# Kernel optimization log

Measured on AMD Instinct MI355X. Metric: run time of the kernel, lower is better.

## Reference

```python
import jax, jax.numpy as jnp
import numpy as np

B, N, K, D = 256, 100, 16, 128


def setup_inputs() -> dict:
    key = jax.random.key(0)
    k1, k2, k3, k4, k5, k6, k7 = jax.random.split(key, 7)
    return {
        "self_vectors": jax.random.normal(k1, (B, N, D), jnp.float32),
        "neighbor_vector": jax.random.normal(k2, (B, N, K, D), jnp.float32),
        "neighbor_weight": jax.random.uniform(k3, (B, N, K), jnp.float32),
        "extra_vector": jax.random.normal(k4, (B, N, D), jnp.float32),
        "w_1": jax.random.normal(k5, (D + 1, D), jnp.float32) / np.sqrt(D + 1),
        "w_2": jax.random.normal(k6, (D, 1), jnp.float32) / np.sqrt(D),
        "w_3": jax.random.normal(k7, (2 * D, D), jnp.float32) / np.sqrt(2 * D),
        "batch_size": B,
    }


def reference(self_vectors, neighbor_vector, neighbor_weight, extra_vector, w_1, w_2, w_3, batch_size):
    # attention branch (extra_vector is not None)
    feat = extra_vector[:, :, None, :] * neighbor_vector           # [B,N,K,D]
    feat = jnp.concatenate([feat, neighbor_weight[..., None]], -1)  # [B,N,K,D+1]
    alpha = jnp.einsum('bnkf,fd->bnkd', feat, w_1)                  # [B,N,K,D]
    alpha = jax.nn.leaky_relu(alpha, negative_slope=0.2)
    alpha = jnp.einsum('bnkd,do->bnk', alpha, w_2)                  # [B,N,K]
    alpha = jax.nn.softmax(alpha, axis=-1)[..., None]               # [B,N,K,1]
    agg = jnp.sum(alpha * neighbor_vector, axis=-2)                 # [B,N,D]
    # combine (dropout is identity in eval mode / p=0)
    out = jnp.concatenate([self_vectors, agg], axis=-1) @ w_3       # [B,N,D]
    out = out.reshape(batch_size, -1, w_3.shape[1])
    return jax.nn.relu(out)
```

## Files before the change

### kernel.cpp

```cpp
#include <hip/hip_runtime.h>
#include <stdint.h>

#define BN_TOTAL 25600
#define DDIM 128
#define KN 16

typedef __bf16 bf16x8 __attribute__((ext_vector_type(8)));
typedef __bf16 bf16x4 __attribute__((ext_vector_type(4)));
typedef float f32x4 __attribute__((ext_vector_type(4)));
typedef float f32x16 __attribute__((ext_vector_type(16)));

__device__ __forceinline__ void gload_lds16(const void* g, void* l) {
    __builtin_amdgcn_global_load_lds(
        (const __attribute__((address_space(1))) void*)g,
        (__attribute__((address_space(3))) void*)l, 16, 0, 0);
}

template<int CTRL>
__device__ __forceinline__ float rotadd(float v) {
    const int r = __builtin_amdgcn_mov_dpp(__builtin_bit_cast(int, v), CTRL, 0xF, 0xF, false);
    return v + __builtin_bit_cast(float, r);
}
__device__ __forceinline__ float allreduce16(float v) {
    v = rotadd<0x121>(v);
    v = rotadd<0x122>(v);
    v = rotadd<0x124>(v);
    v = rotadd<0x128>(v);
    return v;
}

__global__ __launch_bounds__(256) void k0_build_frags(
    const float* __restrict__ w1,
    const float* __restrict__ w3,
    bf16x8* __restrict__ fw1,
    bf16x8* __restrict__ fw3)
{
    const int slot = blockIdx.x * 256 + threadIdx.x;
    if (slot < 2048) {
        const int idx  = slot >> 6;
        const int lane = slot & 63;
        const int t = idx >> 2, s = idx & 3;
        const int grp = lane >> 4, lr = lane & 15;
        const int fbase = grp * 8 + 32 * s;
        const int d = t * 16 + lr;
        bf16x8 tmp;
        #pragma unroll
        for (int j = 0; j < 8; ++j)
            tmp[j] = (__bf16)w1[(fbase + j) * DDIM + d];
        fw1[slot] = tmp;
    } else {
        const int q = slot - 2048;
        const int idx  = q >> 6;
        const int lane = q & 63;
        const int t = idx >> 3, s = idx & 7;
        const int grp = lane >> 4, lr = lane & 15;
        const int fbase = grp * 8 + 32 * s;
        const int d = t * 16 + lr;
        bf16x8 tmp;
        #pragma unroll
        for (int j = 0; j < 8; ++j)
            tmp[j] = (__bf16)w3[(fbase + j) * DDIM + d];
        fw3[q] = tmp;
    }
}

__global__ __launch_bounds__(512, 6) void k1_attn_agg(
    const float* __restrict__ nbr,
    const float* __restrict__ wgt,
    const float* __restrict__ extra,
    const float* __restrict__ w1,
    const float* __restrict__ w2,
    const bf16x8* __restrict__ fw1,
    unsigned short* __restrict__ aggb)
{
    __shared__ bf16x8 b1frag[32][64];
    __shared__ float2 wlw2[DDIM];
    __shared__ __align__(16) unsigned short alds[8][16];

    const int tid  = threadIdx.x;
    const int lane = tid & 63;
    const int wave = tid >> 6;
    const int grp  = lane >> 4;
    const int lr   = lane & 15;
    const int half = lane >> 5;
    const int col  = lane & 31;

    #pragma unroll
    for (int c = 0; c < 4; ++c)
        gload_lds16(fw1 + (wave * 4 + c) * 64 + lane, &b1frag[wave * 4 + c][0]);
    if (tid < DDIM)
        wlw2[tid] = make_float2(w1[DDIM * DDIM + tid], w2[tid]);
    __syncthreads();

    const int bn = blockIdx.x * 8 + wave;
    const float* nb = nbr   + (size_t)bn * (KN * DDIM);
    const float* ex = extra + (size_t)bn * DDIM;

    const float4 wv = *(const float4*)(wgt + (size_t)bn * KN + grp * 4);
    float w2v[8];
    f32x4 acc[8];
    #pragma unroll
    for (int t = 0; t < 8; ++t) {
        const float2 ww = wlw2[t * 16 + lr];
        w2v[t] = ww.y;
        acc[t][0] = wv.x * ww.x;
        acc[t][1] = wv.y * ww.x;
        acc[t][2] = wv.z * ww.x;
        acc[t][3] = wv.w * ww.x;
    }

    #pragma unroll
    for (int s = 0; s < 4; ++s) {
        const int f0 = grp * 8 + 32 * s;
        const float4 n0 = *(const float4*)(nb + lr * DDIM + f0);
        const float4 n1 = *(const float4*)(nb + lr * DDIM + f0 + 4);
        const float4 e0 = *(const float4*)(ex + f0);
        const float4 e1 = *(const float4*)(ex + f0 + 4);
        bf16x8 af;
        af[0] = (__bf16)(n0.x * e0.x); af[1] = (__bf16)(n0.y * e0.y);
        af[2] = (__bf16)(n0.z * e0.z); af[3] = (__bf16)(n0.w * e0.w);
        af[4] = (__bf16)(n1.x * e1.x); af[5] = (__bf16)(n1.y * e1.y);
        af[6] = (__bf16)(n1.z * e1.z); af[7] = (__bf16)(n1.w * e1.w);
        #pragma unroll
        for (int t = 0; t < 8; ++t)
            acc[t] = __builtin_amdgcn_mfma_f32_16x16x32_bf16(
                         af, b1frag[t * 4 + s][lane], acc[t], 0, 0, 0);
    }

    bf16x8 b2f[4];
    #pragma unroll
    for (int t = 0; t < 4; ++t)
        #pragma unroll
        for (int j = 0; j < 8; ++j)
            b2f[t][j] = (__bf16)nb[(half * 8 + j) * DDIM + t * 32 + col];

    float sum0 = 0.f, sum1 = 0.f, sum2 = 0.f, sum3 = 0.f;
    #pragma unroll
    for (int t = 0; t < 8; ++t) {
        float h;
        h = acc[t][0]; h = fmaxf(h, 0.2f * h); sum0 = fmaf(h, w2v[t], sum0);
        h = acc[t][1]; h = fmaxf(h, 0.2f * h); sum1 = fmaf(h, w2v[t], sum1);
        h = acc[t][2]; h = fmaxf(h, 0.2f * h); sum2 = fmaf(h, w2v[t], sum2);
        h = acc[t][3]; h = fmaxf(h, 0.2f * h); sum3 = fmaf(h, w2v[t], sum3);
    }
    sum0 = allreduce16(sum0);
    sum1 = allreduce16(sum1);
    sum2 = allreduce16(sum2);
    sum3 = allreduce16(sum3);

    float mx = fmaxf(fmaxf(sum0, sum1), fmaxf(sum2, sum3));
    mx = fmaxf(mx, __shfl_xor(mx, 16, 64));
    mx = fmaxf(mx, __shfl_xor(mx, 32, 64));
    const float ev0 = __expf(sum0 - mx);
    const float ev1 = __expf(sum1 - mx);
    const float ev2 = __expf(sum2 - mx);
    const float ev3 = __expf(sum3 - mx);
    float es = ev0 + ev1 + ev2 + ev3;
    es += __shfl_xor(es, 16, 64);
    es += __shfl_xor(es, 32, 64);
    const float inv = 1.0f / es;

    if (lr == 0) {
        bf16x4 av;
        av[0] = (__bf16)(ev0 * inv);
        av[1] = (__bf16)(ev1 * inv);
        av[2] = (__bf16)(ev2 * inv);
        av[3] = (__bf16)(ev3 * inv);
        *(bf16x4*)&alds[wave][grp * 4] = av;
    }
    const bf16x8 a2 = *(const bf16x8*)&alds[wave][half * 8];

    f32x16 z;
    #pragma unroll
    for (int i = 0; i < 16; ++i) z[i] = 0.f;

    unsigned short* ao = aggb + (size_t)bn * DDIM;
    #pragma unroll
    for (int t = 0; t < 4; ++t) {
        const f32x16 r = __builtin_amdgcn_mfma_f32_32x32x16_bf16(a2, b2f[t], z, 0, 0, 0);
        if ((t >> 1) == half) {
            const __bf16 rb = (__bf16)r[0];
            ao[t * 32 + col] = __builtin_bit_cast(unsigned short, rb);
        }
    }
}

__global__ __launch_bounds__(512, 4) void k2_out_gemm(
    const float* __restrict__ selfv,
    const unsigned short* __restrict__ aggb,
    const bf16x8* __restrict__ fw3,
    float* __restrict__ out)
{
    __shared__ bf16x8 w3frag[64][64];

    const int tid  = threadIdx.x;
    const int lane = tid & 63;
    const int wave = tid >> 6;
    const int grp  = lane >> 4;
    const int lr   = lane & 15;

    #pragma unroll
    for (int c = 0; c < 8; ++c)
        gload_lds16(fw3 + (wave * 8 + c) * 64 + lane, &w3frag[wave * 8 + c][0]);
    __syncthreads();

    const int rowbase = blockIdx.x * 128 + wave * 16;
    const int row = rowbase + lr;

    f32x4 acc[8];
    #pragma unroll
    for (int t = 0; t < 8; ++t) {
        acc[t][0] = 0.f; acc[t][1] = 0.f; acc[t][2] = 0.f; acc[t][3] = 0.f;
    }

    #pragma unroll
    for (int s = 0; s < 8; ++s) {
        bf16x8 af;
        if (s < 4) {
            const int f0 = grp * 8 + 32 * s;
            const float4 x0 = *(const float4*)(selfv + (size_t)row * DDIM + f0);
            const float4 x1 = *(const float4*)(selfv + (size_t)row * DDIM + f0 + 4);
            af[0] = (__bf16)x0.x; af[1] = (__bf16)x0.y;
            af[2] = (__bf16)x0.z; af[3] = (__bf16)x0.w;
            af[4] = (__bf16)x1.x; af[5] = (__bf16)x1.y;
            af[6] = (__bf16)x1.z; af[7] = (__bf16)x1.w;
        } else {
            const int f0 = grp * 8 + 32 * (s - 4);
            af = *(const bf16x8*)(aggb + (size_t)row * DDIM + f0);
        }
        #pragma unroll
        for (int t = 0; t < 8; ++t)
            acc[t] = __builtin_amdgcn_mfma_f32_16x16x32_bf16(
                         af, w3frag[t * 8 + s][lane], acc[t], 0, 0, 0);
    }

    #pragma unroll
    for (int t = 0; t < 8; ++t) {
        #pragma unroll
        for (int j = 0; j < 4; ++j) {
            const int r = rowbase + grp * 4 + j;
            out[(size_t)r * DDIM + t * 16 + lr] = fmaxf(acc[t][j], 0.0f);
        }
    }
}

extern "C" void kernel_launch(void* const* d_in, const int* in_sizes, int n_in,
                              void* d_out, int out_size, void* d_ws, size_t ws_size,
                              hipStream_t stream)
{
    const float* selfv = (const float*)d_in[0];
    const float* nbr   = (const float*)d_in[1];
    const float* wgt   = (const float*)d_in[2];
    const float* extra = (const float*)d_in[3];
    const float* w1    = (const float*)d_in[4];
    const float* w2    = (const float*)d_in[5];
    const float* w3    = (const float*)d_in[6];
    float* out = (float*)d_out;

    unsigned short* aggb = (unsigned short*)d_ws;
    bf16x8* fw1 = (bf16x8*)((char*)d_ws + (8u << 20));
    bf16x8* fw3 = (bf16x8*)((char*)d_ws + (8u << 20) + (128u << 10));

    hipLaunchKernelGGL(k0_build_frags, dim3(24), dim3(256), 0, stream, w1, w3, fw1, fw3);
    hipLaunchKernelGGL(k1_attn_agg, dim3(3200), dim3(512), 0, stream,
                       nbr, wgt, extra, w1, w2, fw1, aggb);
    hipLaunchKernelGGL(k2_out_gemm, dim3(200), dim3(512), 0, stream,
                       selfv, aggb, fw3, out);
}
```

Before: 72.85 us.

## Fuse output GEMM into attention-aggregation kernel via LDS staging

Merges the attention/aggregation kernel and the output GEMM into one kernel. Each block now keeps its 8 aggregated rows in LDS and runs the concat-GEMM with w3 directly, so the bf16 agg round trip through global memory and one launch go away. In exchange, each wave loads w3 fragments from global into registers, and the 16x16 MFMA handles only 8 valid rows, so half of its output is wasted. Launch bounds drop from 6 to 4 waves-per-EU occupancy, which may reduce latency hiding for the memory-bound neighbor loads.

```diff
diff --git a/kernel.cpp b/kernel.cpp
--- a/kernel.cpp
+++ b/kernel.cpp
@@ -4,6 +4,7 @@
 #define BN_TOTAL 25600
 #define DDIM 128
 #define KN 16
+#define AGP 136
 
 typedef __bf16 bf16x8 __attribute__((ext_vector_type(8)));
 typedef __bf16 bf16x4 __attribute__((ext_vector_type(4)));
@@ -64,18 +65,21 @@
     }
 }
 
-__global__ __launch_bounds__(512, 6) void k1_attn_agg(
+__global__ __launch_bounds__(512, 4) void k_fused(
     const float* __restrict__ nbr,
     const float* __restrict__ wgt,
     const float* __restrict__ extra,
     const float* __restrict__ w1,
     const float* __restrict__ w2,
+    const float* __restrict__ selfv,
     const bf16x8* __restrict__ fw1,
-    unsigned short* __restrict__ aggb)
+    const bf16x8* __restrict__ fw3,
+    float* __restrict__ out)
 {
     __shared__ bf16x8 b1frag[32][64];
     __shared__ float2 wlw2[DDIM];
     __shared__ __align__(16) unsigned short alds[8][16];
+    __shared__ __align__(16) unsigned short agg_lds[8][AGP];
 
     const int tid  = threadIdx.x;
     const int lane = tid & 63;
@@ -92,7 +96,8 @@
         wlw2[tid] = make_float2(w1[DDIM * DDIM + tid], w2[tid]);
     __syncthreads();
 
-    const int bn = blockIdx.x * 8 + wave;
+    const int bn8 = blockIdx.x * 8;
+    const int bn  = bn8 + wave;
     const float* nb = nbr   + (size_t)bn * (KN * DDIM);
     const float* ex = extra + (size_t)bn * DDIM;
 
@@ -174,72 +179,57 @@
     #pragma unroll
     for (int i = 0; i < 16; ++i) z[i] = 0.f;
 
-    unsigned short* ao = aggb + (size_t)bn * DDIM;
     #pragma unroll
     for (int t = 0; t < 4; ++t) {
         const f32x16 r = __builtin_amdgcn_mfma_f32_32x32x16_bf16(a2, b2f[t], z, 0, 0, 0);
         if ((t >> 1) == half) {
             const __bf16 rb = (__bf16)r[0];
-            ao[t * 32 + col] = __builtin_bit_cast(unsigned short, rb);
+            agg_lds[wave][t * 32 + col] = __builtin_bit_cast(unsigned short, rb);
         }
     }
-}
-
-__global__ __launch_bounds__(512, 4) void k2_out_gemm(
-    const float* __restrict__ selfv,
-    const unsigned short* __restrict__ aggb,
-    const bf16x8* __restrict__ fw3,
-    float* __restrict__ out)
-{
-    __shared__ bf16x8 w3frag[64][64];
-
-    const int tid  = threadIdx.x;
-    const int lane = tid & 63;
-    const int wave = tid >> 6;
-    const int grp  = lane >> 4;
-    const int lr   = lane & 15;
-
-    #pragma unroll
-    for (int c = 0; c < 8; ++c)
-        gload_lds16(fw3 + (wave * 8 + c) * 64 + lane, &w3frag[wave * 8 + c][0]);
+
+    const int arow = lane & 7;
+    const int kofs = grp * 8;
+    float4 sx[4][2];
+    #pragma unroll
+    for (int s = 0; s < 4; ++s) {
+        const float* sp = selfv + (size_t)(bn8 + arow) * DDIM + kofs + 32 * s;
+        sx[s][0] = *(const float4*)sp;
+        sx[s][1] = *(const float4*)(sp + 4);
+    }
+    bf16x8 wf[8];
+    {
+        const bf16x8* fp = fw3 + (size_t)(wave * 8) * 64 + lane;
+        #pragma unroll
+        for (int s = 0; s < 8; ++s)
+            wf[s] = fp[s * 64];
+    }
+
     __syncthreads();
 
-    const int rowbase = blockIdx.x * 128 + wave * 16;
-    const int row = rowbase + lr;
-
-    f32x4 acc[8];
-    #pragma unroll
-    for (int t = 0; t < 8; ++t) {
-        acc[t][0] = 0.f; acc[t][1] = 0.f; acc[t][2] = 0.f; acc[t][3] = 0.f;
-    }
-
-    #pragma unroll
-    for (int s = 0; s < 8; ++s) {
+    f32x4 acc2;
+    acc2[0] = 0.f; acc2[1] = 0.f; acc2[2] = 0.f; acc2[3] = 0.f;
+
+    #pragma unroll
+    for (int s = 0; s < 4; ++s) {
         bf16x8 af;
-        if (s < 4) {
-            const int f0 = grp * 8 + 32 * s;
-            const float4 x0 = *(const float4*)(selfv + (size_t)row * DDIM + f0);
-            const float4 x1 = *(const float4*)(selfv + (size_t)row * DDIM + f0 + 4);
-            af[0] = (__bf16)x0.x; af[1] = (__bf16)x0.y;
-            af[2] = (__bf16)x0.z; af[3] = (__bf16)x0.w;
-            af[4] = (__bf16)x1.x; af[5] = (__bf16)x1.y;
-            af[6] = (__bf16)x1.z; af[7] = (__bf16)x1.w;
-        } else {
-            const int f0 = grp * 8 + 32 * (s - 4);
-            af = *(const bf16x8*)(aggb + (size_t)row * DDIM + f0);
-        }
-        #pragma unroll
-        for (int t = 0; t < 8; ++t)
-            acc[t] = __builtin_amdgcn_mfma_f32_16x16x32_bf16(
-                         af, w3frag[t * 8 + s][lane], acc[t], 0, 0, 0);
-    }
-
-    #pragma unroll
-    for (int t = 0; t < 8; ++t) {
+        af[0] = (__bf16)sx[s][0].x; af[1] = (__bf16)sx[s][0].y;
+        af[2] = (__bf16)sx[s][0].z; af[3] = (__bf16)sx[s][0].w;
+        af[4] = (__bf16)sx[s][1].x; af[5] = (__bf16)sx[s][1].y;
+        af[6] = (__bf16)sx[s][1].z; af[7] = (__bf16)sx[s][1].w;
+        acc2 = __builtin_amdgcn_mfma_f32_16x16x32_bf16(af, wf[s], acc2, 0, 0, 0);
+    }
+    #pragma unroll
+    for (int s = 0; s < 4; ++s) {
+        const bf16x8 af = *(const bf16x8*)&agg_lds[arow][kofs + 32 * s];
+        acc2 = __builtin_amdgcn_mfma_f32_16x16x32_bf16(af, wf[4 + s], acc2, 0, 0, 0);
+    }
+
+    if (grp < 2) {
         #pragma unroll
         for (int j = 0; j < 4; ++j) {
-            const int r = rowbase + grp * 4 + j;
-            out[(size_t)r * DDIM + t * 16 + lr] = fmaxf(acc[t][j], 0.0f);
+            const int r = bn8 + grp * 4 + j;
+            out[(size_t)r * DDIM + wave * 16 + lr] = fmaxf(acc2[j], 0.0f);
         }
     }
 }
@@ -257,13 +247,10 @@
     const float* w3    = (const float*)d_in[6];
     float* out = (float*)d_out;
 
-    unsigned short* aggb = (unsigned short*)d_ws;
     bf16x8* fw1 = (bf16x8*)((char*)d_ws + (8u << 20));
     bf16x8* fw3 = (bf16x8*)((char*)d_ws + (8u << 20) + (128u << 10));
 
     hipLaunchKernelGGL(k0_build_frags, dim3(24), dim3(256), 0, stream, w1, w3, fw1, fw3);
-    hipLaunchKernelGGL(k1_attn_agg, dim3(3200), dim3(512), 0, stream,
-                       nbr, wgt, extra, w1, w2, fw1, aggb);
-    hipLaunchKernelGGL(k2_out_gemm, dim3(200), dim3(512), 0, stream,
-                       selfv, aggb, fw3, out);
-}
+    hipLaunchKernelGGL(k_fused, dim3(3200), dim3(512), 0, stream,
+                       nbr, wgt, extra, w1, w2, selfv, fw1, fw3, out);
+}
```

Measured after the change: 83.73 us. 1.15x slower.

## Pipeline neighbor tiles through double-buffered LDS with async global-to-LDS loads

Applied to the files above, without the earlier changes.

The attention kernel becomes persistent-style: each 2-wave block handles 10 (b,n) rows per wave and prefetches the next rows' neighbor, extra and weight data into a double-buffered, XOR-swizzled LDS buffer using async global_load_lds, gated by explicit vmcnt waits. The goal is to overlap the dominant HBM streaming of neighbor vectors with the MFMA and softmax work, where the old version issued dependent global loads per row. W1 fragments are now read straight from global memory (cache) rather than staged in LDS. The risks are fewer waves for latency hiding, correctness of the hand-written vmcnt counts, and the repeated global reads of fw1 fragments.

```diff
diff --git a/kernel.cpp b/kernel.cpp
--- a/kernel.cpp
+++ b/kernel.cpp
@@ -4,6 +4,7 @@
 #define BN_TOTAL 25600
 #define DDIM 128
 #define KN 16
+#define K1_ITERS 10
 
 typedef __bf16 bf16x8 __attribute__((ext_vector_type(8)));
 typedef __bf16 bf16x4 __attribute__((ext_vector_type(4)));
@@ -64,7 +65,7 @@
     }
 }
 
-__global__ __launch_bounds__(512, 6) void k1_attn_agg(
+__global__ __launch_bounds__(128) void k1_pipe(
     const float* __restrict__ nbr,
     const float* __restrict__ wgt,
     const float* __restrict__ extra,
@@ -73,9 +74,9 @@
     const bf16x8* __restrict__ fw1,
     unsigned short* __restrict__ aggb)
 {
-    __shared__ bf16x8 b1frag[32][64];
+    __shared__ float buf[2][2][2304];
     __shared__ float2 wlw2[DDIM];
-    __shared__ __align__(16) unsigned short alds[8][16];
+    __shared__ __align__(16) unsigned short alds[2][16];
 
     const int tid  = threadIdx.x;
     const int lane = tid & 63;
@@ -85,104 +86,132 @@
     const int half = lane >> 5;
     const int col  = lane & 31;
 
-    #pragma unroll
-    for (int c = 0; c < 4; ++c)
-        gload_lds16(fw1 + (wave * 4 + c) * 64 + lane, &b1frag[wave * 4 + c][0]);
-    if (tid < DDIM)
-        wlw2[tid] = make_float2(w1[DDIM * DDIM + tid], w2[tid]);
+    const int bnbase = blockIdx.x * (2 * K1_ITERS) + wave * K1_ITERS;
+
+    #define STAGE(IT, PHASE)                                                   \
+    {                                                                          \
+        const int bn_ = bnbase + (IT);                                         \
+        const float* nb_ = nbr + (size_t)bn_ * (KN * DDIM);                    \
+        float* dst_ = &buf[(PHASE)][wave][0];                                  \
+        _Pragma("unroll")                                                      \
+        for (int i_ = 0; i_ < 8; ++i_) {                                       \
+            const int r_ = 2 * i_ + (lane >> 5);                               \
+            const int c_ = (lane & 31) ^ (r_ & 7);                             \
+            gload_lds16(nb_ + r_ * DDIM + c_ * 4, dst_ + i_ * 256);            \
+        }                                                                      \
+        const float* ex_ = extra + (size_t)bn_ * DDIM;                         \
+        const float* wg_ = wgt + (size_t)bn_ * KN;                             \
+        const float* sr_ = (lane < 32) ? (ex_ + (lane & 31) * 4)               \
+                          : (lane < 36) ? (wg_ + (lane - 32) * 4) : ex_;       \
+        gload_lds16(sr_, dst_ + 2048);                                         \
+    }
+
+    STAGE(0, 0)
+    STAGE(1, 1)
+    wlw2[tid] = make_float2(w1[DDIM * DDIM + tid], w2[tid]);
     __syncthreads();
 
-    const int bn = blockIdx.x * 8 + wave;
-    const float* nb = nbr   + (size_t)bn * (KN * DDIM);
-    const float* ex = extra + (size_t)bn * DDIM;
-
-    const float4 wv = *(const float4*)(wgt + (size_t)bn * KN + grp * 4);
-    float w2v[8];
-    f32x4 acc[8];
-    #pragma unroll
-    for (int t = 0; t < 8; ++t) {
-        const float2 ww = wlw2[t * 16 + lr];
-        w2v[t] = ww.y;
-        acc[t][0] = wv.x * ww.x;
-        acc[t][1] = wv.y * ww.x;
-        acc[t][2] = wv.z * ww.x;
-        acc[t][3] = wv.w * ww.x;
-    }
-
-    #pragma unroll
-    for (int s = 0; s < 4; ++s) {
-        const int f0 = grp * 8 + 32 * s;
-        const float4 n0 = *(const float4*)(nb + lr * DDIM + f0);
-        const float4 n1 = *(const float4*)(nb + lr * DDIM + f0 + 4);
-        const float4 e0 = *(const float4*)(ex + f0);
-        const float4 e1 = *(const float4*)(ex + f0 + 4);
-        bf16x8 af;
-        af[0] = (__bf16)(n0.x * e0.x); af[1] = (__bf16)(n0.y * e0.y);
-        af[2] = (__bf16)(n0.z * e0.z); af[3] = (__bf16)(n0.w * e0.w);
-        af[4] = (__bf16)(n1.x * e1.x); af[5] = (__bf16)(n1.y * e1.y);
-        af[6] = (__bf16)(n1.z * e1.z); af[7] = (__bf16)(n1.w * e1.w);
-        #pragma unroll
-        for (int t = 0; t < 8; ++t)
-            acc[t] = __builtin_amdgcn_mfma_f32_16x16x32_bf16(
-                         af, b1frag[t * 4 + s][lane], acc[t], 0, 0, 0);
-    }
-
-    bf16x8 b2f[4];
-    #pragma unroll
-    for (int t = 0; t < 4; ++t)
-        #pragma unroll
-        for (int j = 0; j < 8; ++j)
-            b2f[t][j] = (__bf16)nb[(half * 8 + j) * DDIM + t * 32 + col];
-
-    float sum0 = 0.f, sum1 = 0.f, sum2 = 0.f, sum3 = 0.f;
-    #pragma unroll
-    for (int t = 0; t < 8; ++t) {
-        float h;
-        h = acc[t][0]; h = fmaxf(h, 0.2f * h); sum0 = fmaf(h, w2v[t], sum0);
-        h = acc[t][1]; h = fmaxf(h, 0.2f * h); sum1 = fmaf(h, w2v[t], sum1);
-        h = acc[t][2]; h = fmaxf(h, 0.2f * h); sum2 = fmaf(h, w2v[t], sum2);
-        h = acc[t][3]; h = fmaxf(h, 0.2f * h); sum3 = fmaf(h, w2v[t], sum3);
-    }
-    sum0 = allreduce16(sum0);
-    sum1 = allreduce16(sum1);
-    sum2 = allreduce16(sum2);
-    sum3 = allreduce16(sum3);
-
-    float mx = fmaxf(fmaxf(sum0, sum1), fmaxf(sum2, sum3));
-    mx = fmaxf(mx, __shfl_xor(mx, 16, 64));
-    mx = fmaxf(mx, __shfl_xor(mx, 32, 64));
-    const float ev0 = __expf(sum0 - mx);
-    const float ev1 = __expf(sum1 - mx);
-    const float ev2 = __expf(sum2 - mx);
-    const float ev3 = __expf(sum3 - mx);
-    float es = ev0 + ev1 + ev2 + ev3;
-    es += __shfl_xor(es, 16, 64);
-    es += __shfl_xor(es, 32, 64);
-    const float inv = 1.0f / es;
-
-    if (lr == 0) {
-        bf16x4 av;
-        av[0] = (__bf16)(ev0 * inv);
-        av[1] = (__bf16)(ev1 * inv);
-        av[2] = (__bf16)(ev2 * inv);
-        av[3] = (__bf16)(ev3 * inv);
-        *(bf16x4*)&alds[wave][grp * 4] = av;
-    }
-    const bf16x8 a2 = *(const bf16x8*)&alds[wave][half * 8];
-
-    f32x16 z;
-    #pragma unroll
-    for (int i = 0; i < 16; ++i) z[i] = 0.f;
-
-    unsigned short* ao = aggb + (size_t)bn * DDIM;
-    #pragma unroll
-    for (int t = 0; t < 4; ++t) {
-        const f32x16 r = __builtin_amdgcn_mfma_f32_32x32x16_bf16(a2, b2f[t], z, 0, 0, 0);
-        if ((t >> 1) == half) {
-            const __bf16 rb = (__bf16)r[0];
-            ao[t * 32 + col] = __builtin_bit_cast(unsigned short, rb);
-        }
-    }
+    for (int it = 0; it < K1_ITERS; ++it) {
+        if (it + 1 < K1_ITERS) asm volatile("s_waitcnt vmcnt(9)" ::: "memory");
+        else                   asm volatile("s_waitcnt vmcnt(0)" ::: "memory");
+
+        const float* bb = &buf[it & 1][wave][0];
+        const int bn = bnbase + it;
+
+        const float4 wv = *(const float4*)(bb + 2048 + 128 + grp * 4);
+        float w2v[8];
+        f32x4 acc[8];
+        #pragma unroll
+        for (int t = 0; t < 8; ++t) {
+            const float2 ww = wlw2[t * 16 + lr];
+            w2v[t] = ww.y;
+            acc[t][0] = wv.x * ww.x;
+            acc[t][1] = wv.y * ww.x;
+            acc[t][2] = wv.z * ww.x;
+            acc[t][3] = wv.w * ww.x;
+        }
+
+        #pragma unroll
+        for (int s = 0; s < 4; ++s) {
+            const int c0 = grp * 2 + 8 * s;
+            const float4 n0 = *(const float4*)(bb + lr * DDIM + ((c0    ) ^ (lr & 7)) * 4);
+            const float4 n1 = *(const float4*)(bb + lr * DDIM + ((c0 + 1) ^ (lr & 7)) * 4);
+            const float4 e0 = *(const float4*)(bb + 2048 + grp * 8 + 32 * s);
+            const float4 e1 = *(const float4*)(bb + 2048 + grp * 8 + 32 * s + 4);
+            bf16x8 af;
+            af[0] = (__bf16)(n0.x * e0.x); af[1] = (__bf16)(n0.y * e0.y);
+            af[2] = (__bf16)(n0.z * e0.z); af[3] = (__bf16)(n0.w * e0.w);
+            af[4] = (__bf16)(n1.x * e1.x); af[5] = (__bf16)(n1.y * e1.y);
+            af[6] = (__bf16)(n1.z * e1.z); af[7] = (__bf16)(n1.w * e1.w);
+            #pragma unroll
+            for (int t = 0; t < 8; ++t)
+                acc[t] = __builtin_amdgcn_mfma_f32_16x16x32_bf16(
+                             af, fw1[(t * 4 + s) * 64 + lane], acc[t], 0, 0, 0);
+        }
+
+        bf16x8 b2f[4];
+        #pragma unroll
+        for (int t = 0; t < 4; ++t)
+            #pragma unroll
+            for (int j = 0; j < 8; ++j) {
+                const int k = half * 8 + j;
+                const int cc = (t * 8 + (col >> 2)) ^ (k & 7);
+                b2f[t][j] = (__bf16)bb[k * DDIM + cc * 4 + (col & 3)];
+            }
+
+        float sum0 = 0.f, sum1 = 0.f, sum2 = 0.f, sum3 = 0.f;
+        #pragma unroll
+        for (int t = 0; t < 8; ++t) {
+            float h;
+            h = acc[t][0]; h = fmaxf(h, 0.2f * h); sum0 = fmaf(h, w2v[t], sum0);
+            h = acc[t][1]; h = fmaxf(h, 0.2f * h); sum1 = fmaf(h, w2v[t], sum1);
+            h = acc[t][2]; h = fmaxf(h, 0.2f * h); sum2 = fmaf(h, w2v[t], sum2);
+            h = acc[t][3]; h = fmaxf(h, 0.2f * h); sum3 = fmaf(h, w2v[t], sum3);
+        }
+        sum0 = allreduce16(sum0);
+        sum1 = allreduce16(sum1);
+        sum2 = allreduce16(sum2);
+        sum3 = allreduce16(sum3);
+
+        float mx = fmaxf(fmaxf(sum0, sum1), fmaxf(sum2, sum3));
+        mx = fmaxf(mx, __shfl_xor(mx, 16, 64));
+        mx = fmaxf(mx, __shfl_xor(mx, 32, 64));
+        const float ev0 = __expf(sum0 - mx);
+        const float ev1 = __expf(sum1 - mx);
+        const float ev2 = __expf(sum2 - mx);
+        const float ev3 = __expf(sum3 - mx);
+        float es = ev0 + ev1 + ev2 + ev3;
+        es += __shfl_xor(es, 16, 64);
+        es += __shfl_xor(es, 32, 64);
+        const float inv = 1.0f / es;
+
+        if (lr == 0) {
+            bf16x4 av;
+            av[0] = (__bf16)(ev0 * inv);
+            av[1] = (__bf16)(ev1 * inv);
+            av[2] = (__bf16)(ev2 * inv);
+            av[3] = (__bf16)(ev3 * inv);
+            *(bf16x4*)&alds[wave][grp * 4] = av;
+        }
+        const bf16x8 a2 = *(const bf16x8*)&alds[wave][half * 8];
+
+        f32x16 z;
+        #pragma unroll
+        for (int i = 0; i < 16; ++i) z[i] = 0.f;
+
+        unsigned short* ao = aggb + (size_t)bn * DDIM;
+        #pragma unroll
+        for (int t = 0; t < 4; ++t) {
+            const f32x16 r = __builtin_amdgcn_mfma_f32_32x32x16_bf16(a2, b2f[t], z, 0, 0, 0);
+            if ((t >> 1) == half) {
+                const __bf16 rb = (__bf16)r[0];
+                ao[t * 32 + col] = __builtin_bit_cast(unsigned short, rb);
+            }
+        }
+
+        if (it + 2 < K1_ITERS) STAGE(it + 2, it & 1)
+    }
+    #undef STAGE
 }
 
 __global__ __launch_bounds__(512, 4) void k2_out_gemm(
@@ -262,7 +291,7 @@
     bf16x8* fw3 = (bf16x8*)((char*)d_ws + (8u << 20) + (128u << 10));
 
     hipLaunchKernelGGL(k0_build_frags, dim3(24), dim3(256), 0, stream, w1, w3, fw1, fw3);
-    hipLaunchKernelGGL(k1_attn_agg, dim3(3200), dim3(512), 0, stream,
+    hipLaunchKernelGGL(k1_pipe, dim3(1280), dim3(128), 0, stream,
                        nbr, wgt, extra, w1, w2, fw1, aggb);
     hipLaunchKernelGGL(k2_out_gemm, dim3(200), dim3(512), 0, stream,
                        selfv, aggb, fw3, out);
```

After: 128.4 us. +76.3%, slower.
